# Kernel tuning notes

Measured on AMD Instinct MI355X. Metric: run time of the kernel, lower is better.

The kernel has to match this reference:

```python
import jax, jax.numpy as jnp
import numpy as np

N, n, m, k = 100000, 32, 16, 32
MU = 100.0  # bubble kernel scale (init arg mu)


def setup_inputs() -> dict:
    key = jax.random.key(0)
    ks = jax.random.split(key, 7)
    x = jax.random.normal(ks[0], (N,), dtype=jnp.float32)
    # torch.nn.Linear(N, n): weight [n, N], bias [n]
    encoder_w = jax.random.normal(ks[1], (n, N), dtype=jnp.float32) / np.float32(np.sqrt(N))
    encoder_b = jnp.zeros((n,), dtype=jnp.float32)
    # decoder parameter [n, N]
    decoder = jax.random.normal(ks[2], (n, N), dtype=jnp.float32) / np.float32(np.sqrt(n))
    # torch.nn.Linear(n, n*m): weight [n*m, n], bias [n*m]
    bw_w = jax.random.normal(ks[3], (n * m, n), dtype=jnp.float32) / np.float32(np.sqrt(n))
    bw_b = jnp.zeros((n * m,), dtype=jnp.float32)
    neighbour_distance = jax.random.uniform(ks[4], (N, k), dtype=jnp.float32)
    neighbour_id = jax.random.randint(ks[5], (N, k), 0, N)
    clustering_labels = jax.random.randint(ks[6], (N,), 0, m)
    return {
        "x": x,
        "encoder_w": encoder_w,
        "encoder_b": encoder_b,
        "decoder": decoder,
        "bw_w": bw_w,
        "bw_b": bw_b,
        "neighbour_distance": neighbour_distance,
        "neighbour_id": neighbour_id,
        "clustering_labels": clustering_labels,
    }


def reference(x, encoder_w, encoder_b, decoder, bw_w, bw_b,
              neighbour_distance, neighbour_id, clustering_labels):
    # encode: [N] -> [n]
    encoded = x @ encoder_w.T + encoder_b
    # per-basis, per-cluster bandwidths: sigmoid(Linear)/60 -> [n, m] -> expand to [n, N]
    bandwidths = jax.nn.sigmoid(encoded @ bw_w.T + bw_b) / 60.0
    w = bandwidths.reshape(n, m)[:, clustering_labels]  # [n, N]
    # bubble window: relu(1 - d^2 / (w*mu)^2) -> [n, N, k]
    window = jax.nn.relu(1.0 - neighbour_distance[None, :, :] ** 2
                         / (w[:, :, None] * MU) ** 2)
    # normalization over axis 1 (the N axis), faithful to the source's dim=1
    window = window / jnp.sum(window, axis=1, keepdims=True)
    # gather decoder rows at neighbours, weight, reduce over k: [n, N]
    convolved_basis = jnp.sum(decoder[:, neighbour_id] * window, axis=-1)
    # [n] @ [n, N] -> [N]
    return encoded @ convolved_basis
```

## Files before the change

kernel.cpp:

```cpp
#include <hip/hip_runtime.h>
#include <hip/hip_fp16.h>

#define N_PTS 100000
#define MU_F  100.0f

typedef unsigned int uint;
typedef _Float16 h2 __attribute__((ext_vector_type(2)));
typedef float f2 __attribute__((ext_vector_type(2)));

#define E_SCALE 16384.0f
#define E_SCALE_INV (1.0f / 16384.0f)

static __device__ inline h2 h2pack(float a, float b) {
    return __builtin_bit_cast(h2, __builtin_amdgcn_cvt_pkrtz(a, b));
}
static __device__ inline float fdot2f(h2 a, h2 b, float c) {
    return __builtin_amdgcn_fdot2(a, b, c, false);
}
static __device__ inline h2 h2fma(h2 a, h2 b, h2 c) {
#if __has_builtin(__builtin_elementwise_fma)
    return __builtin_elementwise_fma(a, b, c);
#else
    return a * b + c;
#endif
}
static __device__ inline h2 h2max(h2 a, h2 b) {
#if __has_builtin(__builtin_elementwise_max)
    return __builtin_elementwise_max(a, b);
#else
    h2 r;
    r.x = a.x > b.x ? a.x : b.x;
    r.y = a.y > b.y ? a.y : b.y;
    return r;
#endif
}

#define ENC_BLKS 256
#define TR_BLKS  1563
#define S_BLKS   1024
#define NPAIRS   (N_PTS / 2)
#define S_CH     ((NPAIRS + S_BLKS - 1) / S_BLKS)
#define M_BLKS   1024
#define M_CH     ((NPAIRS + M_BLKS - 1) / M_BLKS)

__global__ __launch_bounds__(256) void k_prep(const float* __restrict__ x,
                                              const float* __restrict__ encW,
                                              const float* __restrict__ encB,
                                              float* __restrict__ enc) {
    int b = blockIdx.x;
    int row = b & 31;
    int chunk = b >> 5;
    const int CH = N_PTS / 8;
    int base = chunk * CH;
    const float4* W4 = reinterpret_cast<const float4*>(encW + (size_t)row * N_PTS + base);
    const float4* x4 = reinterpret_cast<const float4*>(x + base);
    const int nv = CH / 4;
    float acc = 0.f;
    for (int idx = threadIdx.x; idx < nv; idx += 256) {
        float4 w = W4[idx];
        float4 xv = x4[idx];
        acc += w.x * xv.x + w.y * xv.y + w.z * xv.z + w.w * xv.w;
    }
    #pragma unroll
    for (int off = 32; off > 0; off >>= 1) acc += __shfl_down(acc, off);
    __shared__ float sred[4];
    int wid = threadIdx.x >> 6;
    if ((threadIdx.x & 63) == 0) sred[wid] = acc;
    __syncthreads();
    if (threadIdx.x == 0) {
        float s = sred[0] + sred[1] + sred[2] + sred[3];
        if (chunk == 0) s += encB[row];
        atomicAdd(enc + row, s);
    }
}

__device__ inline void build_invF(const float* __restrict__ encL,
                                  const float* __restrict__ bw_w,
                                  const float* __restrict__ bw_b,
                                  float* __restrict__ invF) {
    for (int r = threadIdx.x; r < 512; r += 256) {
        int i = r >> 4, c = r & 15;
        float z = bw_b[r];
        const float* wr = bw_w + r * 32;
        #pragma unroll
        for (int p = 0; p < 32; ++p) z = fmaf(encL[p], wr[p], z);
        float s = 1.f / (1.f + __expf(-z));
        float wmu = s * (MU_F / 60.0f);
        invF[c * 32 + i] = 1.f / (wmu * wmu);
    }
}

__global__ __launch_bounds__(256, 4) void k_S(const float* __restrict__ enc_g,
                                              const float* __restrict__ bw_w,
                                              const float* __restrict__ bw_b,
                                              const float* __restrict__ nd,
                                              const int* __restrict__ labels,
                                              float* __restrict__ S,
                                              float* __restrict__ S_part,
                                              const float* __restrict__ dec,
                                              __half* __restrict__ decT) {
    int b = blockIdx.x;
    if (b >= S_BLKS) {
        __shared__ float tile[32][65];
        int j0 = (b - S_BLKS) * 64;
        int col = threadIdx.x & 63;
        int r0 = threadIdx.x >> 6;
        #pragma unroll
        for (int it = 0; it < 8; ++it) {
            int row = it * 4 + r0;
            int j = j0 + col;
            float v = (j < N_PTS) ? dec[(size_t)row * N_PTS + j] : 0.f;
            tile[row][col] = v;
        }
        __syncthreads();
        #pragma unroll
        for (int it = 0; it < 4; ++it) {
            int idx = it * 256 + threadIdx.x;
            int j = idx >> 4;
            int p = idx & 15;
            int jj = j0 + j;
            if (jj < N_PTS) {
                __half2 h = __halves2half2(__float2half(tile[2 * p][j]),
                                           __float2half(tile[2 * p + 1][j]));
                *reinterpret_cast<__half2*>(decT + (size_t)jj * 32 + 2 * p) = h;
            }
        }
        return;
    }

    __shared__ float encL[32];
    __shared__ float invF[512];
    __shared__ float Sloc[1024];
    if (threadIdx.x < 32) encL[threadIdx.x] = enc_g[threadIdx.x];
    for (int t = threadIdx.x; t < 1024; t += 256) Sloc[t] = 0.f;
    __syncthreads();
    build_invF(encL, bw_w, bw_b, invF);
    __syncthreads();

    int lane = threadIdx.x & 63;
    int kk = lane & 31;
    int jh = lane >> 5;
    int w = threadIdx.x >> 6;
    int start = b * S_CH;
    int pend = min(start + S_CH, NPAIRS);
    int p = start + w;

    f2 acc2[16];
    #pragma unroll
    for (int t = 0; t < 16; ++t) { acc2[t].x = 0.f; acc2[t].y = 0.f; }

    if (p < pend) {
        auto ld = [&](int pc, float& d, int& c) {
            pc = min(pc, NPAIRS - 1);
            int j = 2 * pc + jh;
            d = nd[(size_t)j * 32 + kk];
            c = labels[j];
        };
        float dA, dB; int cA, cB;
        ld(p, dA, cA);
        ld(p + 4, dB, cB);
        f2 onev; onev.x = 1.f; onev.y = 1.f;
        while (p < pend) {
            float dC; int cC;
            ld(p + 8, dC, cC);
            float d2 = dA * dA;
            f2 md2; md2.x = -d2; md2.y = -d2;
            const float4* ivp = reinterpret_cast<const float4*>(&invF[cA * 32]);
            #pragma unroll
            for (int t4 = 0; t4 < 8; ++t4) {
                float4 iv = ivp[t4];
                f2 i01; i01.x = iv.x; i01.y = iv.y;
                f2 i23; i23.x = iv.z; i23.y = iv.w;
                f2 w0 = md2 * i01 + onev;
                w0.x = fmaxf(w0.x, 0.f);
                w0.y = fmaxf(w0.y, 0.f);
                acc2[2 * t4] += w0;
                f2 w1 = md2 * i23 + onev;
                w1.x = fmaxf(w1.x, 0.f);
                w1.y = fmaxf(w1.y, 0.f);
                acc2[2 * t4 + 1] += w1;
            }
            dA = dB; cA = cB; dB = dC; cB = cC;
            p += 4;
        }
    }
    #pragma unroll
    for (int t = 0; t < 16; ++t) {
        acc2[t].x += __shfl_xor(acc2[t].x, 32);
        acc2[t].y += __shfl_xor(acc2[t].y, 32);
    }
    if (jh == 0) {
        #pragma unroll
        for (int t = 0; t < 16; ++t) {
            atomicAdd(&Sloc[(2 * t) * 32 + kk], acc2[t].x);
            atomicAdd(&Sloc[(2 * t + 1) * 32 + kk], acc2[t].y);
        }
    }
    __syncthreads();
    if (S_part) {
        for (int t = threadIdx.x; t < 1024; t += 256)
            S_part[(size_t)b * 1024 + t] = Sloc[t];
    } else {
        for (int t = threadIdx.x; t < 1024; t += 256) {
            float v = Sloc[t];
            if (v != 0.f) atomicAdd(&S[t], v);
        }
    }
}

__global__ __launch_bounds__(1024) void k_S_reduce(const float* __restrict__ S_part,
                                                   float* __restrict__ S) {
    int g = blockIdx.x;
    int t = threadIdx.x;
    float s = 0.f;
    #pragma unroll
    for (int u = 0; u < 16; ++u)
        s += S_part[(size_t)(g * 16 + u) * 1024 + t];
    atomicAdd(&S[t], s);
}

__global__ __launch_bounds__(256, 4) void k_main(const float* __restrict__ enc_g,
                                                 const float* __restrict__ bw_w,
                                                 const float* __restrict__ bw_b,
                                                 const float* __restrict__ S_g,
                                                 const float* __restrict__ nd,
                                                 const int* __restrict__ nid,
                                                 const int* __restrict__ labels,
                                                 const __half* __restrict__ decT,
                                                 float* __restrict__ out) {
    __shared__ float encL[32];
    __shared__ float invF[512];
    __shared__ float ELf[1024];
    __shared__ h2 invHL[256];

    if (threadIdx.x < 32) encL[threadIdx.x] = enc_g[threadIdx.x];
    __syncthreads();
    build_invF(encL, bw_w, bw_b, invF);
    for (int t = threadIdx.x; t < 1024; t += 256)
        ELf[t] = encL[t >> 5] / S_g[t] * E_SCALE;
    __syncthreads();
    {
        int t = threadIdx.x;
        int c = t >> 4, q = (t >> 2) & 3, tt = t & 3;
        int i0 = q * 8 + 2 * tt;
        invHL[t] = h2pack(fminf(invF[c * 32 + i0], 6.0e4f),
                          fminf(invF[c * 32 + i0 + 1], 6.0e4f));
    }
    __syncthreads();

    int lane = threadIdx.x & 63;
    int R = lane >> 2;
    int q = lane & 3;

    h2 EhA[4], EhB[4];
    #pragma unroll
    for (int t = 0; t < 4; ++t) {
        int i0 = q * 8 + 2 * t;
        EhA[t] = h2pack(ELf[i0 * 32 + R], ELf[(i0 + 1) * 32 + R]);
        EhB[t] = h2pack(ELf[i0 * 32 + R + 16], ELf[(i0 + 1) * 32 + R + 16]);
    }
    const h2 zero2 = h2pack(0.f, 0.f);
    const h2 one2 = h2pack(1.f, 1.f);

    int w = threadIdx.x >> 6;
    int start = blockIdx.x * M_CH;
    int pend = min(start + M_CH, NPAIRS);
    int pa = start + w;
    const uint4* decQ = reinterpret_cast<const uint4*>(decT);
    if (pa >= pend) return;

    auto load_ldd = [&](int pc, int* id, float* dd, int& c0, int& c1) {
        pc = min(pc, NPAIRS - 1);
        int j0 = 2 * pc, j1 = j0 + 1;
        #pragma unroll
        for (int s = 0; s < 4; ++s) {
            size_t idx = (size_t)((s >> 1) ? j1 : j0) * 32 + (s & 1) * 16 + R;
            id[s] = nid[idx];
            dd[s] = nd[idx];
        }
        c0 = labels[j0];
        c1 = labels[j1];
    };
    auto load_rows = [&](const int* id, uint4* r) {
        #pragma unroll
        for (int s = 0; s < 4; ++s)
            r[s] = decQ[(size_t)id[s] * 4 + q];
    };
    auto load_ih = [&](int c0, int c1, h2* ih0, h2* ih1) {
        uint4 a = *reinterpret_cast<const uint4*>(&invHL[c0 * 16 + q * 4]);
        uint4 bq = *reinterpret_cast<const uint4*>(&invHL[c1 * 16 + q * 4]);
        ih0[0] = __builtin_bit_cast(h2, a.x);  ih0[1] = __builtin_bit_cast(h2, a.y);
        ih0[2] = __builtin_bit_cast(h2, a.z);  ih0[3] = __builtin_bit_cast(h2, a.w);
        ih1[0] = __builtin_bit_cast(h2, bq.x); ih1[1] = __builtin_bit_cast(h2, bq.y);
        ih1[2] = __builtin_bit_cast(h2, bq.z); ih1[3] = __builtin_bit_cast(h2, bq.w);
    };

    int ida[4], idb[4]; float dda[4], ddb[4];
    int ca0, ca1, cb0, cb1;
    uint4 ra[4], rb[4];
    h2 ihA0[4], ihA1[4];

    load_ldd(pa, ida, dda, ca0, ca1);
    load_ldd(pa + 4, idb, ddb, cb0, cb1);
    load_rows(ida, ra);
    load_ih(ca0, ca1, ihA0, ihA1);

    while (pa < pend) {
        load_rows(idb, rb);
        h2 ihB0[4], ihB1[4];
        load_ih(cb0, cb1, ihB0, ihB1);
        int idc[4]; float ddc[4]; int cc0, cc1;
        load_ldd(pa + 8, idc, ddc, cc0, cc1);

        float d20 = dda[0] * dda[0];
        float d21 = dda[1] * dda[1];
        float d22 = dda[2] * dda[2];
        float d23 = dda[3] * dda[3];
        h2 md0 = h2pack(-d20, -d20);
        h2 md1 = h2pack(-d21, -d21);
        h2 md2 = h2pack(-d22, -d22);
        h2 md3 = h2pack(-d23, -d23);

        float a0 = 0.f, a1 = 0.f, a2 = 0.f, a3 = 0.f;
        #pragma unroll
        for (int t = 0; t < 4; ++t) {
            uint dw0 = (t == 0) ? ra[0].x : (t == 1) ? ra[0].y : (t == 2) ? ra[0].z : ra[0].w;
            uint dw1 = (t == 0) ? ra[1].x : (t == 1) ? ra[1].y : (t == 2) ? ra[1].z : ra[1].w;
            uint dw2 = (t == 0) ? ra[2].x : (t == 1) ? ra[2].y : (t == 2) ? ra[2].z : ra[2].w;
            uint dw3 = (t == 0) ? ra[3].x : (t == 1) ? ra[3].y : (t == 2) ? ra[3].z : ra[3].w;
            {
                h2 wv = h2max(h2fma(md0, ihA0[t], one2), zero2);
                a0 = fdot2f(wv * EhA[t], __builtin_bit_cast(h2, dw0), a0);
            }
            {
                h2 wv = h2max(h2fma(md1, ihA0[t], one2), zero2);
                a1 = fdot2f(wv * EhB[t], __builtin_bit_cast(h2, dw1), a1);
            }
            {
                h2 wv = h2max(h2fma(md2, ihA1[t], one2), zero2);
                a2 = fdot2f(wv * EhA[t], __builtin_bit_cast(h2, dw2), a2);
            }
            {
                h2 wv = h2max(h2fma(md3, ihA1[t], one2), zero2);
                a3 = fdot2f(wv * EhB[t], __builtin_bit_cast(h2, dw3), a3);
            }
        }
        float u = a0 + a1;
        float v = a2 + a3;
        #pragma unroll
        for (int off = 32; off > 0; off >>= 1) {
            u += __shfl_xor(u, off);
            v += __shfl_xor(v, off);
        }
        if (lane == 0)  out[2 * pa]     = u * E_SCALE_INV;
        if (lane == 32) out[2 * pa + 1] = v * E_SCALE_INV;

        ca0 = cb0; ca1 = cb1; cb0 = cc0; cb1 = cc1;
        #pragma unroll
        for (int s = 0; s < 4; ++s) {
            dda[s] = ddb[s]; ddb[s] = ddc[s];
            ida[s] = idb[s]; idb[s] = idc[s];
            ra[s] = rb[s];
            ihA0[s] = ihB0[s]; ihA1[s] = ihB1[s];
        }
        pa += 4;
    }
}

extern "C" void kernel_launch(void* const* d_in, const int* in_sizes, int n_in,
                              void* d_out, int out_size, void* d_ws, size_t ws_size,
                              hipStream_t stream) {
    const float* x     = (const float*)d_in[0];
    const float* enc_w = (const float*)d_in[1];
    const float* enc_b = (const float*)d_in[2];
    const float* dec   = (const float*)d_in[3];
    const float* bw_w  = (const float*)d_in[4];
    const float* bw_b  = (const float*)d_in[5];
    const float* nd    = (const float*)d_in[6];
    const int*   nid   = (const int*)d_in[7];
    const int*   labels= (const int*)d_in[8];
    float* out = (float*)d_out;

    char* ws = (char*)d_ws;
    float* enc    = (float*)(ws + 0);
    float* S      = (float*)(ws + 128);
    __half* decT  = (__half*)(ws + 532480);
    bool use_part = ws_size >= 11126784ull;
    float* S_part = use_part ? (float*)(ws + 6932480) : nullptr;

    (void)hipMemsetAsync(d_ws, 0, 4224, stream);
    k_prep<<<dim3(ENC_BLKS), dim3(256), 0, stream>>>(x, enc_w, enc_b, enc);
    k_S<<<dim3(S_BLKS + TR_BLKS), dim3(256), 0, stream>>>(
        enc, bw_w, bw_b, nd, labels, S, S_part, dec, decT);
    if (use_part)
        k_S_reduce<<<dim3(64), dim3(1024), 0, stream>>>(S_part, S);
    k_main<<<dim3(M_BLKS), dim3(256), 0, stream>>>(enc, bw_w, bw_b, S, nd, nid,
                                                   labels, decT, out);
}
```

Baseline: 190.9 us.

## Unroll S-kernel loop by four pairs, add nontemporal loads and more main blocks

The window-sum kernel now processes four point pairs per iteration. It batch-loads distances and labels 16 pairs ahead, masks out-of-range entries with a huge distance so they contribute zero, and uses vector max. Distance and id loads in both kernels become nontemporal, and sched barriers keep the prefetch loads ahead of compute. The main kernel's block count doubles to raise parallelism. This is meant to expose more memory-level parallelism and hide load latency, at the cost of more registers and possibly lower occupancy.

```diff
diff --git a/kernel.cpp b/kernel.cpp
--- a/kernel.cpp
+++ b/kernel.cpp
@@ -34,13 +34,23 @@
     return r;
 #endif
 }
+static __device__ inline f2 f2max(f2 a, f2 b) {
+#if __has_builtin(__builtin_elementwise_max)
+    return __builtin_elementwise_max(a, b);
+#else
+    f2 r;
+    r.x = fmaxf(a.x, b.x);
+    r.y = fmaxf(a.y, b.y);
+    return r;
+#endif
+}
 
 #define ENC_BLKS 256
 #define TR_BLKS  1563
 #define S_BLKS   1024
 #define NPAIRS   (N_PTS / 2)
 #define S_CH     ((NPAIRS + S_BLKS - 1) / S_BLKS)
-#define M_BLKS   1024
+#define M_BLKS   2048
 #define M_CH     ((NPAIRS + M_BLKS - 1) / M_BLKS)
 
 __global__ __launch_bounds__(256) void k_prep(const float* __restrict__ x,
@@ -150,38 +160,46 @@
     for (int t = 0; t < 16; ++t) { acc2[t].x = 0.f; acc2[t].y = 0.f; }
 
     if (p < pend) {
-        auto ld = [&](int pc, float& d, int& c) {
-            pc = min(pc, NPAIRS - 1);
-            int j = 2 * pc + jh;
-            d = nd[(size_t)j * 32 + kk];
-            c = labels[j];
+        auto ld4 = [&](int pbase, float* d, int* cc) {
+            #pragma unroll
+            for (int u = 0; u < 4; ++u) {
+                int pc = pbase + 4 * u;
+                int pcl = min(pc, NPAIRS - 1);
+                int j = 2 * pcl + jh;
+                float dv = __builtin_nontemporal_load(&nd[(size_t)j * 32 + kk]);
+                cc[u] = labels[j];
+                d[u] = (pc < pend) ? dv : 1.0e15f;
+            }
         };
-        float dA, dB; int cA, cB;
-        ld(p, dA, cA);
-        ld(p + 4, dB, cB);
+        float dA[4], dB[4]; int cA[4], cB[4];
+        ld4(p, dA, cA);
         f2 onev; onev.x = 1.f; onev.y = 1.f;
+        f2 zero2f; zero2f.x = 0.f; zero2f.y = 0.f;
         while (p < pend) {
-            float dC; int cC;
-            ld(p + 8, dC, cC);
-            float d2 = dA * dA;
-            f2 md2; md2.x = -d2; md2.y = -d2;
-            const float4* ivp = reinterpret_cast<const float4*>(&invF[cA * 32]);
+            ld4(p + 16, dB, cB);
+            __builtin_amdgcn_sched_barrier(0);
+            f2 md[4];
+            const float4* ivp[4];
+            #pragma unroll
+            for (int u = 0; u < 4; ++u) {
+                float d2 = dA[u] * dA[u];
+                md[u].x = -d2; md[u].y = -d2;
+                ivp[u] = reinterpret_cast<const float4*>(&invF[cA[u] * 32]);
+            }
             #pragma unroll
             for (int t4 = 0; t4 < 8; ++t4) {
-                float4 iv = ivp[t4];
-                f2 i01; i01.x = iv.x; i01.y = iv.y;
-                f2 i23; i23.x = iv.z; i23.y = iv.w;
-                f2 w0 = md2 * i01 + onev;
-                w0.x = fmaxf(w0.x, 0.f);
-                w0.y = fmaxf(w0.y, 0.f);
-                acc2[2 * t4] += w0;
-                f2 w1 = md2 * i23 + onev;
-                w1.x = fmaxf(w1.x, 0.f);
-                w1.y = fmaxf(w1.y, 0.f);
-                acc2[2 * t4 + 1] += w1;
-            }
-            dA = dB; cA = cB; dB = dC; cB = cC;
-            p += 4;
+                #pragma unroll
+                for (int u = 0; u < 4; ++u) {
+                    float4 iv = ivp[u][t4];
+                    f2 i01; i01.x = iv.x; i01.y = iv.y;
+                    f2 i23; i23.x = iv.z; i23.y = iv.w;
+                    acc2[2 * t4]     += f2max(md[u] * i01 + onev, zero2f);
+                    acc2[2 * t4 + 1] += f2max(md[u] * i23 + onev, zero2f);
+                }
+            }
+            #pragma unroll
+            for (int u = 0; u < 4; ++u) { dA[u] = dB[u]; cA[u] = cB[u]; }
+            p += 16;
         }
     }
     #pragma unroll
@@ -275,8 +293,8 @@
         #pragma unroll
         for (int s = 0; s < 4; ++s) {
             size_t idx = (size_t)((s >> 1) ? j1 : j0) * 32 + (s & 1) * 16 + R;
-            id[s] = nid[idx];
-            dd[s] = nd[idx];
+            id[s] = __builtin_nontemporal_load(&nid[idx]);
+            dd[s] = __builtin_nontemporal_load(&nd[idx]);
         }
         c0 = labels[j0];
         c1 = labels[j1];
@@ -311,6 +329,7 @@
         load_ih(cb0, cb1, ihB0, ihB1);
         int idc[4]; float ddc[4]; int cc0, cc1;
         load_ldd(pa + 8, idc, ddc, cc0, cc1);
+        __builtin_amdgcn_sched_barrier(0);
 
         float d20 = dda[0] * dda[0];
         float d21 = dda[1] * dda[1];
```

New measurement: 203.8 us. 1.07x slower.
